# Optimization experiments

Hardware: AMD Instinct MI355X
Metric: run time of the kernel (lower is better)

Reference implementation:

```python
import jax, jax.numpy as jnp
import numpy as np

B, N, F_IN = 8, 1024, 64
HEADS = 8
D = F_IN  # out_features per head (in_features == out_features)


def setup_inputs() -> dict:
    key = jax.random.key(0)
    ks = jax.random.split(key, 5)
    stdv = 1.0 / np.sqrt(F_IN * HEADS)
    h = jax.random.normal(ks[0], (B, N, F_IN), dtype=jnp.float32)
    adj = jnp.ones((B, N, N), dtype=jnp.float32)  # passed but unused by the module
    W = jax.random.uniform(ks[1], (F_IN, D * HEADS), minval=-stdv, maxval=stdv, dtype=jnp.float32)
    a = jax.random.uniform(ks[2], (2 * D, 1), minval=-stdv, maxval=stdv, dtype=jnp.float32)
    out_W = jax.random.normal(ks[3], (D * HEADS, F_IN), dtype=jnp.float32) / np.sqrt(D * HEADS)
    out_b = jnp.zeros((F_IN,), dtype=jnp.float32)
    return {"h": h, "adj": adj, "W": W, "a": a, "out_W": out_W, "out_b": out_b}


def reference(h, adj, W, a, out_W, out_b):
    Bv, Nv, _ = h.shape
    Dh = W.shape[1] // HEADS
    # Wh: [B, N, H, D]
    Wh = (h @ W).reshape(Bv, Nv, HEADS, Dh)
    # Additive attention decomposed: e[b,i,j,h] = leaky_relu(Wh[b,i,h].a_src + Wh[b,j,h].a_dst)
    a_src = jnp.einsum('bnhd,d->bnh', Wh, a[:Dh, 0])
    a_dst = jnp.einsum('bnhd,d->bnh', Wh, a[Dh:, 0])
    e = jax.nn.leaky_relu(a_src[:, :, None, :] + a_dst[:, None, :, :], negative_slope=0.01)  # [B,N,N,H]
    # Module applies softmax over dim=1 (the first node axis i)
    attn = jax.nn.softmax(e, axis=1)  # [B,N,N,H]
    # h_prime[b,i,h,:] = sum_j attn[b,i,j,h] * Wh[b,j,h,:]
    h_prime = jnp.einsum('bijh,bjhd->bihd', attn, Wh).reshape(Bv, Nv, HEADS * Dh)
    return h_prime @ out_W + out_b
```

## Files before the change

kernel.cpp:

```cpp
#include <hip/hip_runtime.h>


#define B_  8
#define N_  1024
#define H_  8
#define D_  64
#define BH_ 64
#define CH_ 32
#define CL_ 32

__device__ __forceinline__ float bcast_lane(float v, int l) {
  return __int_as_float(__builtin_amdgcn_readlane(__float_as_int(v), l));
}

__global__ __launch_bounds__(256) void k_wh(
    const float* __restrict__ h, const float* __restrict__ W,
    const float* __restrict__ a,
    float* __restrict__ Wh, float* __restrict__ sArr, float* __restrict__ tArr) {
  __shared__ float whL[16 * 512];
  __shared__ float aL[128];
  const int tid = threadIdx.x;
  const int lane = tid & 63;
  const int row0 = blockIdx.x * 16;
  const int b = row0 >> 10;
  if (tid < 128) aL[tid] = a[tid];

  float hreg[16];
#pragma unroll
  for (int r = 0; r < 16; ++r) hreg[r] = h[(row0 + r) * 64 + lane];

  float acc0[16], acc1[16];
#pragma unroll
  for (int r = 0; r < 16; ++r) { acc0[r] = 0.f; acc1[r] = 0.f; }
#pragma unroll 4
  for (int k = 0; k < 64; ++k) {
    const float w0 = W[k * 512 + tid];
    const float w1 = W[k * 512 + tid + 256];
#pragma unroll
    for (int r = 0; r < 16; ++r) {
      const float hv = bcast_lane(hreg[r], k);
      acc0[r] += hv * w0;
      acc1[r] += hv * w1;
    }
  }
  const int hh0 = tid >> 6, d0 = tid & 63;
  const int hh1 = (tid + 256) >> 6;
#pragma unroll
  for (int r = 0; r < 16; ++r) {
    const int n = (row0 + r) & (N_ - 1);
    whL[r * 512 + tid] = acc0[r];
    whL[r * 512 + tid + 256] = acc1[r];
    Wh[((b * H_ + hh0) * N_ + n) * D_ + d0] = acc0[r];
    Wh[((b * H_ + hh1) * N_ + n) * D_ + d0] = acc1[r];
  }
  __syncthreads();
  if (tid < 128) {
    const int r = tid >> 3, hh = tid & 7;
    const int n = (row0 + r) & (N_ - 1);
    float accS = 0.f, accT = 0.f;
    for (int jj = 0; jj < 64; ++jj) {
      const int d = (jj + tid) & 63;
      const float wv = whL[r * 512 + hh * 64 + d];
      accS += wv * aL[d];
      accT += wv * aL[64 + d];
    }
    sArr[(b * H_ + hh) * N_ + n] = accS;
    tArr[(b * H_ + hh) * N_ + n] = accT;
  }
}

__global__ __launch_bounds__(1024) void k_sort(
    const float* __restrict__ sArr, const float* __restrict__ tArr,
    const float* __restrict__ Wh,
    int* __restrict__ tsi, float* __restrict__ uArr, float* __restrict__ vArr,
    int* __restrict__ qrk,
    float* __restrict__ cOff1, float* __restrict__ cOff2) {
  __shared__ float sL[1024];
  __shared__ float tvL[1024];
  __shared__ int   tiL[1024];
  __shared__ float cum1L[1024], cum001L[1024];
  __shared__ float uL[1024], vL[1024];
  __shared__ float cs1[CH_ * 64], cs2[CH_ * 64];
  __shared__ float ws1[16], ws2[16];
  const int tid = threadIdx.x;
  const int lane = tid & 63;
  const int wv_ = tid >> 6;
  const int bh = blockIdx.x;

  const float orig_s = sArr[bh * N_ + tid];
  float sv_r = orig_s;
  float tv_r = tArr[bh * N_ + tid];
  int   ti_r = tid;

  for (int size = 2; size <= 1024; size <<= 1) {
    for (int stride = size >> 1; stride > 0; stride >>= 1) {
      const bool up = ((tid & size) == 0);
      const bool lower = ((tid & stride) == 0);
      float psv, ptv; int pti;
      if (stride >= 64) {
        sL[tid] = sv_r; tvL[tid] = tv_r; tiL[tid] = ti_r;
        __syncthreads();
        const int p = tid ^ stride;
        psv = sL[p]; ptv = tvL[p]; pti = tiL[p];
        __syncthreads();
      } else {
        psv = __shfl_xor(sv_r, stride);
        ptv = __shfl_xor(tv_r, stride);
        pti = __shfl_xor(ti_r, stride);
      }
      const bool sameDir = (up == lower);
      const bool pLessS = (psv < sv_r);
      if (pLessS == sameDir) sv_r = psv;
      const bool pLessT = (ptv < tv_r) || (ptv == tv_r && pti < ti_r);
      if (pLessT == sameDir) { tv_r = ptv; ti_r = pti; }
    }
  }
  sL[tid] = sv_r; tvL[tid] = tv_r; tiL[tid] = ti_r;

  float c1 = __expf(sv_r) , c001 = __expf(0.01f * sv_r);
  {
    float a1 = c1, a2 = c001;
#pragma unroll
    for (int off = 1; off < 64; off <<= 1) {
      const float x1 = __shfl_up(a1, off);
      const float x2 = __shfl_up(a2, off);
      if (lane >= off) { a1 += x1; a2 += x2; }
    }
    if (lane == 63) { ws1[wv_] = a1; ws2[wv_] = a2; }
    __syncthreads();
    float o1 = 0.f, o2 = 0.f;
    for (int ww = 0; ww < 16; ++ww) {
      if (ww < wv_) { o1 += ws1[ww]; o2 += ws2[ww]; }
    }
    c1 = a1 + o1; c001 = a2 + o2;
  }
  cum1L[tid] = c1; cum001L[tid] = c001;
  __syncthreads();
  const float totalHi = cum1L[1023];

  {
    const float tj = tv_r;
    const float th = -tj;
    int lo = 0, hi = 1024;
    while (lo < hi) { const int mid = (lo + hi) >> 1; if (sL[mid] <= th) lo = mid + 1; else hi = mid; }
    const float S_lo = (lo > 0) ? cum001L[lo - 1] : 0.f;
    const float S_hi = totalHi - ((lo > 0) ? cum1L[lo - 1] : 0.f);
    const float et = __expf(tj), et001 = __expf(0.01f * tj);
    const float Z = et * S_hi + et001 * S_lo;
    const float u = et / Z, v = et001 / Z;
    uL[tid] = u; vL[tid] = v;
    uArr[bh * N_ + tid] = u; vArr[bh * N_ + tid] = v;
    tsi[bh * N_ + tid] = ti_r;
  }

  {
    const float th = -orig_s;
    int lo = 0, hi = 1024;
    while (lo < hi) { const int mid = (lo + hi) >> 1; if (tvL[mid] <= th) lo = mid + 1; else hi = mid; }
    qrk[bh * N_ + tid] = lo;
  }
  __syncthreads();

  const int c = tid >> 6, d = tid & 63;
#pragma unroll
  for (int half = 0; half < 2; ++half) {
    const int cc = c + half * 16;
    float s1 = 0.f, s2 = 0.f;
    for (int k2 = 0; k2 < CL_; ++k2) {
      const int k = cc * CL_ + k2;
      const int j = tiL[k];
      const float w = Wh[(bh * N_ + j) * D_ + d];
      s1 += uL[k] * w;
      s2 += vL[k] * w;
    }
    cs1[cc * 64 + d] = s1; cs2[cc * 64 + d] = s2;
  }
  __syncthreads();
#pragma unroll
  for (int half = 0; half < 2; ++half) {
    const int cc = c + half * 16;
    float o1 = 0.f, o2 = 0.f;
    for (int m = 0; m < cc; ++m) { o1 += cs1[m * 64 + d]; o2 += cs2[m * 64 + d]; }
    cOff1[(bh * CH_ + cc) * 64 + d] = o1;
    cOff2[(bh * CH_ + cc) * 64 + d] = o2;
  }
}

__global__ __launch_bounds__(64) void k_inc(
    const float* __restrict__ Wh, const int* __restrict__ tsi,
    const float* __restrict__ uArr, const float* __restrict__ vArr,
    const float* __restrict__ cOff1, const float* __restrict__ cOff2,
    float* __restrict__ INC1, float* __restrict__ INC2) {
  const int blk = blockIdx.x;
  const int bh = blk >> 5, c = blk & (CH_ - 1);
  const int d = threadIdx.x;
  float r1 = cOff1[blk * 64 + d];
  float r2 = cOff2[blk * 64 + d];
  const int base = bh * N_;
#pragma unroll 8
  for (int k2 = 0; k2 < CL_; ++k2) {
    const int k = c * CL_ + k2;
    const int j = tsi[base + k];
    const float u = uArr[base + k], v = vArr[base + k];
    const float w = Wh[(base + j) * D_ + d];
    r1 += u * w;
    r2 += v * w;
    INC1[(base + k) * D_ + d] = r1;
    INC2[(base + k) * D_ + d] = r2;
  }
}

__global__ __launch_bounds__(512) void k_out(
    const float* __restrict__ sArr, const int* __restrict__ qrk,
    const float* __restrict__ INC1, const float* __restrict__ INC2,
    const float* __restrict__ outW, const float* __restrict__ outb,
    float* __restrict__ out) {
  __shared__ float part[8 * 8 * 64];
  __shared__ int   rkI[16 * 8];
  __shared__ float esL[16 * 8], es001L[16 * 8];
  const int tid = threadIdx.x;
  const int row0 = blockIdx.x * 16;
  const int b = row0 >> 10;
  const int p = tid >> 6;
  const int lane = tid & 63;

  if (tid < 128) {
    const int r = tid >> 3, hh = tid & 7;
    const int bh = b * H_ + hh;
    const int n = (row0 + r) & (N_ - 1);
    const float si = sArr[bh * N_ + n];
    rkI[tid] = qrk[bh * N_ + n];
    esL[tid] = __expf(si);
    es001L[tid] = __expf(0.01f * si);
  }
  __syncthreads();

  float hpv[16];
  {
    const int bh = b * H_ + p;
    const float T1 = INC1[(bh * N_ + (N_ - 1)) * D_ + lane];
#pragma unroll
    for (int r = 0; r < 16; ++r) {
      const int rk = rkI[r * 8 + p];
      float i1 = 0.f, i2 = 0.f;
      if (rk > 0) {
        i1 = INC1[(bh * N_ + rk - 1) * D_ + lane];
        i2 = INC2[(bh * N_ + rk - 1) * D_ + lane];
      }
      hpv[r] = esL[r * 8 + p] * (T1 - i1) + es001L[r * 8 + p] * i2;
    }
  }

  float acc[16];
#pragma unroll
  for (int r = 0; r < 16; ++r) acc[r] = 0.f;
#pragma unroll 4
  for (int kc = 0; kc < 64; ++kc) {
    const float wvv = outW[(p * 64 + kc) * 64 + lane];
#pragma unroll
    for (int r = 0; r < 16; ++r) {
      const float hv = bcast_lane(hpv[r], kc);
      acc[r] += hv * wvv;
    }
  }

  for (int half = 0; half < 2; ++half) {
#pragma unroll
    for (int r = 0; r < 8; ++r) part[(p * 8 + r) * 64 + lane] = acc[half * 8 + r];
    __syncthreads();
    {
      const int r2 = tid >> 6, c2 = tid & 63;
      float ssum = 0.f;
#pragma unroll
      for (int p2 = 0; p2 < 8; ++p2) ssum += part[(p2 * 8 + r2) * 64 + c2];
      out[(row0 + half * 8 + r2) * 64 + c2] = outb[c2] + ssum;
    }
    __syncthreads();
  }
}

extern "C" void kernel_launch(void* const* d_in, const int* in_sizes, int n_in,
                              void* d_out, int out_size, void* d_ws, size_t ws_size,
                              hipStream_t stream) {
  const float* h    = (const float*)d_in[0];
  const float* W    = (const float*)d_in[2];
  const float* a    = (const float*)d_in[3];
  const float* outW = (const float*)d_in[4];
  const float* outb = (const float*)d_in[5];
  float* out = (float*)d_out;

  float* ws   = (float*)d_ws;
  float* Wh   = ws;
  float* sArr = Wh + (size_t)BH_ * N_ * D_;
  float* tArr = sArr + BH_ * N_;
  int*   tsi  = (int*)(tArr + BH_ * N_);
  float* uArr = (float*)(tsi + BH_ * N_);
  float* vArr = uArr + BH_ * N_;
  int*   qrk  = (int*)(vArr + BH_ * N_);
  float* cOff1 = (float*)(qrk + BH_ * N_);
  float* cOff2 = cOff1 + BH_ * CH_ * 64;
  float* INC1 = cOff2 + BH_ * CH_ * 64;
  float* INC2 = INC1 + (size_t)BH_ * N_ * D_;

  hipLaunchKernelGGL(k_wh,   dim3((B_ * N_) / 16), dim3(256), 0, stream,
                     h, W, a, Wh, sArr, tArr);
  hipLaunchKernelGGL(k_sort, dim3(BH_), dim3(1024), 0, stream,
                     sArr, tArr, Wh, tsi, uArr, vArr, qrk, cOff1, cOff2);
  hipLaunchKernelGGL(k_inc,  dim3(BH_ * CH_), dim3(64), 0, stream,
                     Wh, tsi, uArr, vArr, cOff1, cOff2, INC1, INC2);
  hipLaunchKernelGGL(k_out,  dim3((B_ * N_) / 16), dim3(512), 0, stream,
                     sArr, qrk, INC1, INC2, outW, outb, out);
}
```

Measured before the change: 154.9 us.

## Fuse sort and prefix-scan kernels, defer chunk offsets to output kernel

Merges k_sort and k_inc into a single per-(batch,head) kernel. Each wave computes local 32-element inclusive scans of the sorted weighted Wh rows, using readlane broadcasts of indices and weights instead of global tsi/u/v arrays. Chunk prefix offsets are written separately and added back in k_out, which removes one full pass over Wh plus a kernel launch. k_wh also replaces its LDS-based attention dot products with wave shuffle reductions. The trade-off is only 64 blocks doing the scan work, which gives lower parallelism than the previous 2048-block k_inc.

Measured after the change: 160.8 us. 1.04x slower.

```diff
diff --git a/kernel.cpp b/kernel.cpp
--- a/kernel.cpp
+++ b/kernel.cpp
@@ -17,17 +17,17 @@
     const float* __restrict__ h, const float* __restrict__ W,
     const float* __restrict__ a,
     float* __restrict__ Wh, float* __restrict__ sArr, float* __restrict__ tArr) {
-  __shared__ float whL[16 * 512];
-  __shared__ float aL[128];
   const int tid = threadIdx.x;
   const int lane = tid & 63;
+  const int wid = tid >> 6;
   const int row0 = blockIdx.x * 16;
   const int b = row0 >> 10;
-  if (tid < 128) aL[tid] = a[tid];
 
   float hreg[16];
 #pragma unroll
   for (int r = 0; r < 16; ++r) hreg[r] = h[(row0 + r) * 64 + lane];
+  const float a_s = a[lane];
+  const float a_t = a[64 + lane];
 
   float acc0[16], acc1[16];
 #pragma unroll
@@ -43,44 +43,43 @@
       acc1[r] += hv * w1;
     }
   }
-  const int hh0 = tid >> 6, d0 = tid & 63;
-  const int hh1 = (tid + 256) >> 6;
+  const int hh0 = wid, hh1 = wid + 4;
 #pragma unroll
   for (int r = 0; r < 16; ++r) {
     const int n = (row0 + r) & (N_ - 1);
-    whL[r * 512 + tid] = acc0[r];
-    whL[r * 512 + tid + 256] = acc1[r];
-    Wh[((b * H_ + hh0) * N_ + n) * D_ + d0] = acc0[r];
-    Wh[((b * H_ + hh1) * N_ + n) * D_ + d0] = acc1[r];
-  }
-  __syncthreads();
-  if (tid < 128) {
-    const int r = tid >> 3, hh = tid & 7;
+    Wh[((b * H_ + hh0) * N_ + n) * D_ + lane] = acc0[r];
+    Wh[((b * H_ + hh1) * N_ + n) * D_ + lane] = acc1[r];
+  }
+#pragma unroll
+  for (int r = 0; r < 16; ++r) {
     const int n = (row0 + r) & (N_ - 1);
-    float accS = 0.f, accT = 0.f;
-    for (int jj = 0; jj < 64; ++jj) {
-      const int d = (jj + tid) & 63;
-      const float wv = whL[r * 512 + hh * 64 + d];
-      accS += wv * aL[d];
-      accT += wv * aL[64 + d];
-    }
-    sArr[(b * H_ + hh) * N_ + n] = accS;
-    tArr[(b * H_ + hh) * N_ + n] = accT;
-  }
-}
-
-__global__ __launch_bounds__(1024) void k_sort(
+    float s0 = acc0[r] * a_s, t0 = acc0[r] * a_t;
+    float s1 = acc1[r] * a_s, t1 = acc1[r] * a_t;
+#pragma unroll
+    for (int m = 32; m > 0; m >>= 1) {
+      s0 += __shfl_xor(s0, m); t0 += __shfl_xor(t0, m);
+      s1 += __shfl_xor(s1, m); t1 += __shfl_xor(t1, m);
+    }
+    if (lane == 0) {
+      sArr[(b * H_ + hh0) * N_ + n] = s0;
+      tArr[(b * H_ + hh0) * N_ + n] = t0;
+      sArr[(b * H_ + hh1) * N_ + n] = s1;
+      tArr[(b * H_ + hh1) * N_ + n] = t1;
+    }
+  }
+}
+
+__global__ __launch_bounds__(1024) void k_sortinc(
     const float* __restrict__ sArr, const float* __restrict__ tArr,
     const float* __restrict__ Wh,
-    int* __restrict__ tsi, float* __restrict__ uArr, float* __restrict__ vArr,
     int* __restrict__ qrk,
-    float* __restrict__ cOff1, float* __restrict__ cOff2) {
+    float* __restrict__ INC1, float* __restrict__ INC2,
+    float2* __restrict__ cOff) {
   __shared__ float sL[1024];
   __shared__ float tvL[1024];
   __shared__ int   tiL[1024];
   __shared__ float cum1L[1024], cum001L[1024];
-  __shared__ float uL[1024], vL[1024];
-  __shared__ float cs1[CH_ * 64], cs2[CH_ * 64];
+  __shared__ float2 cs12L[CH_ * 64];
   __shared__ float ws1[16], ws2[16];
   const int tid = threadIdx.x;
   const int lane = tid & 63;
@@ -115,9 +114,9 @@
       if (pLessT == sameDir) { tv_r = ptv; ti_r = pti; }
     }
   }
-  sL[tid] = sv_r; tvL[tid] = tv_r; tiL[tid] = ti_r;
-
-  float c1 = __expf(sv_r) , c001 = __expf(0.01f * sv_r);
+  sL[tid] = sv_r; tvL[tid] = tv_r;
+
+  float c1 = __expf(sv_r), c001 = __expf(0.01f * sv_r);
   {
     float a1 = c1, a2 = c001;
 #pragma unroll
@@ -138,6 +137,7 @@
   __syncthreads();
   const float totalHi = cum1L[1023];
 
+  float u_r, v_r;
   {
     const float tj = tv_r;
     const float th = -tj;
@@ -147,10 +147,7 @@
     const float S_hi = totalHi - ((lo > 0) ? cum1L[lo - 1] : 0.f);
     const float et = __expf(tj), et001 = __expf(0.01f * tj);
     const float Z = et * S_hi + et001 * S_lo;
-    const float u = et / Z, v = et001 / Z;
-    uL[tid] = u; vL[tid] = v;
-    uArr[bh * N_ + tid] = u; vArr[bh * N_ + tid] = v;
-    tsi[bh * N_ + tid] = ti_r;
+    u_r = et / Z; v_r = et001 / Z;
   }
 
   {
@@ -159,60 +156,53 @@
     while (lo < hi) { const int mid = (lo + hi) >> 1; if (tvL[mid] <= th) lo = mid + 1; else hi = mid; }
     qrk[bh * N_ + tid] = lo;
   }
-  __syncthreads();
-
-  const int c = tid >> 6, d = tid & 63;
-#pragma unroll
-  for (int half = 0; half < 2; ++half) {
-    const int cc = c + half * 16;
-    float s1 = 0.f, s2 = 0.f;
-    for (int k2 = 0; k2 < CL_; ++k2) {
-      const int k = cc * CL_ + k2;
-      const int j = tiL[k];
-      const float w = Wh[(bh * N_ + j) * D_ + d];
-      s1 += uL[k] * w;
-      s2 += vL[k] * w;
-    }
-    cs1[cc * 64 + d] = s1; cs2[cc * 64 + d] = s2;
-  }
-  __syncthreads();
-#pragma unroll
-  for (int half = 0; half < 2; ++half) {
-    const int cc = c + half * 16;
-    float o1 = 0.f, o2 = 0.f;
-    for (int m = 0; m < cc; ++m) { o1 += cs1[m * 64 + d]; o2 += cs2[m * 64 + d]; }
-    cOff1[(bh * CH_ + cc) * 64 + d] = o1;
-    cOff2[(bh * CH_ + cc) * 64 + d] = o2;
-  }
-}
-
-__global__ __launch_bounds__(64) void k_inc(
-    const float* __restrict__ Wh, const int* __restrict__ tsi,
-    const float* __restrict__ uArr, const float* __restrict__ vArr,
-    const float* __restrict__ cOff1, const float* __restrict__ cOff2,
-    float* __restrict__ INC1, float* __restrict__ INC2) {
-  const int blk = blockIdx.x;
-  const int bh = blk >> 5, c = blk & (CH_ - 1);
-  const int d = threadIdx.x;
-  float r1 = cOff1[blk * 64 + d];
-  float r2 = cOff2[blk * 64 + d];
-  const int base = bh * N_;
+
+  const int d = lane;
+  const int whb = bh * (N_ * D_);
+  const int rbase = bh * N_ + wv_ * 64;
+  float r1 = 0.f, r2 = 0.f;
 #pragma unroll 8
   for (int k2 = 0; k2 < CL_; ++k2) {
-    const int k = c * CL_ + k2;
-    const int j = tsi[base + k];
-    const float u = uArr[base + k], v = vArr[base + k];
-    const float w = Wh[(base + j) * D_ + d];
-    r1 += u * w;
-    r2 += v * w;
-    INC1[(base + k) * D_ + d] = r1;
-    INC2[(base + k) * D_ + d] = r2;
-  }
+    const int   j  = __builtin_amdgcn_readlane(ti_r, k2);
+    const float uu = bcast_lane(u_r, k2);
+    const float vv = bcast_lane(v_r, k2);
+    const float w  = Wh[whb + j * 64 + d];
+    r1 += uu * w; r2 += vv * w;
+    INC1[(rbase + k2) * 64 + d] = r1;
+    INC2[(rbase + k2) * 64 + d] = r2;
+  }
+  const float csA1 = r1, csA2 = r2;
+  r1 = 0.f; r2 = 0.f;
+#pragma unroll 8
+  for (int k2 = 0; k2 < CL_; ++k2) {
+    const int   j  = __builtin_amdgcn_readlane(ti_r, 32 + k2);
+    const float uu = bcast_lane(u_r, 32 + k2);
+    const float vv = bcast_lane(v_r, 32 + k2);
+    const float w  = Wh[whb + j * 64 + d];
+    r1 += uu * w; r2 += vv * w;
+    INC1[(rbase + 32 + k2) * 64 + d] = r1;
+    INC2[(rbase + 32 + k2) * 64 + d] = r2;
+  }
+  cs12L[(2 * wv_) * 64 + d]     = make_float2(csA1, csA2);
+  cs12L[(2 * wv_ + 1) * 64 + d] = make_float2(r1, r2);
+  __syncthreads();
+
+  float o1 = 0.f, o2 = 0.f;
+  for (int m = 0; m < 2 * wv_; ++m) {
+    const float2 cv = cs12L[m * 64 + d];
+    o1 += cv.x; o2 += cv.y;
+  }
+  const int cbase = bh * 33;
+  cOff[(cbase + 2 * wv_) * 64 + d]     = make_float2(o1, o2);
+  cOff[(cbase + 2 * wv_ + 1) * 64 + d] = make_float2(o1 + csA1, o2 + csA2);
+  if (wv_ == 15)
+    cOff[(cbase + 32) * 64 + d] = make_float2(o1 + csA1 + r1, o2 + csA2 + r2);
 }
 
 __global__ __launch_bounds__(512) void k_out(
     const float* __restrict__ sArr, const int* __restrict__ qrk,
     const float* __restrict__ INC1, const float* __restrict__ INC2,
+    const float2* __restrict__ cOff,
     const float* __restrict__ outW, const float* __restrict__ outb,
     float* __restrict__ out) {
   __shared__ float part[8 * 8 * 64];
@@ -238,14 +228,17 @@
   float hpv[16];
   {
     const int bh = b * H_ + p;
-    const float T1 = INC1[(bh * N_ + (N_ - 1)) * D_ + lane];
+    const int cbase = bh * 33;
+    const float T1 = cOff[(cbase + 32) * 64 + lane].x;
 #pragma unroll
     for (int r = 0; r < 16; ++r) {
       const int rk = rkI[r * 8 + p];
       float i1 = 0.f, i2 = 0.f;
       if (rk > 0) {
-        i1 = INC1[(bh * N_ + rk - 1) * D_ + lane];
-        i2 = INC2[(bh * N_ + rk - 1) * D_ + lane];
+        const int idx = rk - 1, cc = idx >> 5;
+        const float2 co = cOff[(cbase + cc) * 64 + lane];
+        i1 = INC1[(bh * N_ + idx) * 64 + lane] + co.x;
+        i2 = INC2[(bh * N_ + idx) * 64 + lane] + co.y;
       }
       hpv[r] = esL[r * 8 + p] * (T1 - i1) + es001L[r * 8 + p] * i2;
     }
@@ -293,21 +286,15 @@
   float* Wh   = ws;
   float* sArr = Wh + (size_t)BH_ * N_ * D_;
   float* tArr = sArr + BH_ * N_;
-  int*   tsi  = (int*)(tArr + BH_ * N_);
-  float* uArr = (float*)(tsi + BH_ * N_);
-  float* vArr = uArr + BH_ * N_;
-  int*   qrk  = (int*)(vArr + BH_ * N_);
-  float* cOff1 = (float*)(qrk + BH_ * N_);
-  float* cOff2 = cOff1 + BH_ * CH_ * 64;
-  float* INC1 = cOff2 + BH_ * CH_ * 64;
+  int*   qrk  = (int*)(tArr + BH_ * N_);
+  float* INC1 = (float*)(qrk + BH_ * N_);
   float* INC2 = INC1 + (size_t)BH_ * N_ * D_;
-
-  hipLaunchKernelGGL(k_wh,   dim3((B_ * N_) / 16), dim3(256), 0, stream,
+  float2* cOff = (float2*)(INC2 + (size_t)BH_ * N_ * D_);
+
+  hipLaunchKernelGGL(k_wh,      dim3((B_ * N_) / 16), dim3(256), 0, stream,
                      h, W, a, Wh, sArr, tArr);
-  hipLaunchKernelGGL(k_sort, dim3(BH_), dim3(1024), 0, stream,
-                     sArr, tArr, Wh, tsi, uArr, vArr, qrk, cOff1, cOff2);
-  hipLaunchKernelGGL(k_inc,  dim3(BH_ * CH_), dim3(64), 0, stream,
-                     Wh, tsi, uArr, vArr, cOff1, cOff2, INC1, INC2);
-  hipLaunchKernelGGL(k_out,  dim3((B_ * N_) / 16), dim3(512), 0, stream,
-                     sArr, qrk, INC1, INC2, outW, outb, out);
-}
+  hipLaunchKernelGGL(k_sortinc, dim3(BH_), dim3(1024), 0, stream,
+                     sArr, tArr, Wh, qrk, INC1, INC2, cOff);
+  hipLaunchKernelGGL(k_out,     dim3((B_ * N_) / 16), dim3(512), 0, stream,
+                     sArr, qrk, INC1, INC2, cOff, outW, outb, out);
+}
```
